# Kernel optimization log

Measured on AMD Instinct MI355X. Metric: run time of the kernel, lower is better.

## Reference

```python
import jax, jax.numpy as jnp
import numpy as np

B, C_IN, H, W = 4, 512, 188, 188
SHARED_CH = 64
NUM_CLASS = 3
M = 200
NUM_MAX = 500
STRIDE = 8
PCR = (-75.2, -75.2, -2.0, 75.2, 75.2, 4.0)
VOX = (0.1, 0.1, 0.15)
OUT_CH = (2, 1, 3, 2, 1, 3)  # center, center_z, dim, rot, iou, hm
MIN_RADIUS = 2.0
OVERLAP = 0.1
INIT_BIAS = -2.19


def conv3x3(x, w):
    return jax.lax.conv_general_dilated(x, w, (1, 1), 'SAME',
                                        dimension_numbers=('NCHW', 'OIHW', 'NCHW'))


def bn_relu(x, p):
    # p: [4, C] = gamma, beta, running_mean, running_var (inference-mode BN)
    g, b, m, v = p[0], p[1], p[2], p[3]
    scale = (g * jax.lax.rsqrt(v + 1e-5))[None, :, None, None]
    y = (x - m[None, :, None, None]) * scale + b[None, :, None, None]
    return jax.nn.relu(y)


def gaussian_radius(height, width, min_overlap):
    # Faithful to OpenPCDet centernet_utils.gaussian_radius
    b1 = height + width
    c1 = width * height * (1 - min_overlap) / (1 + min_overlap)
    sq1 = jnp.sqrt(jnp.maximum(b1 * b1 - 4.0 * c1, 0.0))
    r1 = (b1 + sq1) / 2.0
    b2 = 2.0 * (height + width)
    c2 = (1 - min_overlap) * width * height
    sq2 = jnp.sqrt(jnp.maximum(b2 * b2 - 16.0 * c2, 0.0))
    r2 = (b2 + sq2) / 2.0
    a3 = 4.0 * min_overlap
    b3 = -2.0 * min_overlap * (height + width)
    c3 = (min_overlap - 1.0) * width * height
    sq3 = jnp.sqrt(jnp.maximum(b3 * b3 - 4.0 * a3 * c3, 0.0))
    r3 = (b3 + sq3) / 2.0
    return jnp.minimum(jnp.minimum(r1, r2), r3)


def assign_targets(gt_boxes):
    # gt_boxes: [B, M, 8] = x, y, z, dx, dy, dz, heading, class(1..NUM_CLASS)
    x, y, z = gt_boxes[..., 0], gt_boxes[..., 1], gt_boxes[..., 2]
    dx, dy, dz = gt_boxes[..., 3], gt_boxes[..., 4], gt_boxes[..., 5]
    heading = gt_boxes[..., 6]
    cls = jax.lax.stop_gradient(gt_boxes[..., 7]).astype(jnp.int32)

    cx = jnp.clip((x - PCR[0]) / VOX[0] / STRIDE, 0.0, W - 0.5)  # [B,M]
    cy = jnp.clip((y - PCR[1]) / VOX[1] / STRIDE, 0.0, H - 0.5)
    cxi = jax.lax.stop_gradient(jnp.floor(cx)).astype(jnp.int32)  # .int() trunc == floor (>=0)
    cyi = jax.lax.stop_gradient(jnp.floor(cy)).astype(jnp.int32)

    dxp = dx / VOX[0] / STRIDE
    dyp = dy / VOX[1] / STRIDE
    r = gaussian_radius(dxp, dyp, OVERLAP)
    r = jnp.maximum(jnp.floor(jax.lax.stop_gradient(r)), MIN_RADIUS)  # clamp_min(r.int(), 2)
    sigma = (2.0 * r + 1.0) / 6.0
    valid = (dx > 0) & (dy > 0)  # [B,M]

    ox = jnp.arange(W, dtype=jnp.int32)[None, None, :] - cxi[..., None]  # [B,M,W]
    oy = jnp.arange(H, dtype=jnp.int32)[None, None, :] - cyi[..., None]  # [B,M,H]
    d2 = (oy.astype(jnp.float32) ** 2)[:, :, :, None] + (ox.astype(jnp.float32) ** 2)[:, :, None, :]
    g = jnp.exp(-d2 / (2.0 * sigma * sigma)[:, :, None, None])  # [B,M,H,W]
    win = (jnp.abs(oy)[:, :, :, None] <= r[:, :, None, None]) & \
          (jnp.abs(ox)[:, :, None, :] <= r[:, :, None, None])
    g = jnp.where(win & valid[:, :, None, None], g, 0.0)

    # per-class max-splat (draw_gaussian_to_heatmap uses torch.max overlap)
    heatmap = jnp.stack(
        [jnp.max(jnp.where((cls == c + 1)[:, :, None, None], g, 0.0), axis=1)
         for c in range(NUM_CLASS)], axis=1)  # [B,NUM_CLASS,H,W]

    vf = valid.astype(gt_boxes.dtype)
    vals = jnp.stack([cx - cxi.astype(cx.dtype), cy - cyi.astype(cy.dtype), z,
                      jnp.log(dx), jnp.log(dy), jnp.log(dz),
                      jnp.cos(heading), jnp.sin(heading)], axis=-1) * vf[..., None]
    target_boxes = jnp.zeros((B, NUM_MAX, 8), gt_boxes.dtype).at[:, :M].set(vals)
    ind_vals = (cyi * W + cxi) * valid.astype(jnp.int32)
    inds = jnp.zeros((B, NUM_MAX), jnp.int32).at[:, :M].set(ind_vals)
    mask = jnp.zeros((B, NUM_MAX), jnp.int32).at[:, :M].set(valid.astype(jnp.int32))
    return heatmap, target_boxes, inds, mask


def setup_inputs() -> dict:
    key = jax.random.key(0)
    ks = jax.random.split(key, 16)
    spatial_features = jax.random.normal(ks[0], (B, C_IN, H, W), jnp.float32)
    x = jax.random.uniform(ks[1], (B, M), minval=-70.0, maxval=70.0)
    y = jax.random.uniform(ks[2], (B, M), minval=-70.0, maxval=70.0)
    z = jax.random.uniform(ks[3], (B, M), minval=-1.0, maxval=1.0)
    dx = jax.random.uniform(ks[4], (B, M), minval=1.5, maxval=5.0)
    dy = jax.random.uniform(ks[5], (B, M), minval=1.5, maxval=5.0)
    dz = jax.random.uniform(ks[6], (B, M), minval=1.0, maxval=3.0)
    hd = jax.random.uniform(ks[7], (B, M), minval=-np.pi, maxval=np.pi)
    cls = jax.random.randint(ks[8], (B, M), 1, NUM_CLASS + 1).astype(jnp.float32)
    gt_boxes = jnp.stack([x, y, z, dx, dy, dz, hd, cls], axis=-1)

    def mk_bn(k, lead):
        kk = jax.random.split(k, 4)
        g = 1.0 + 0.1 * jax.random.normal(kk[0], lead + (SHARED_CH,))
        b = 0.1 * jax.random.normal(kk[1], lead + (SHARED_CH,))
        m = 0.1 * jax.random.normal(kk[2], lead + (SHARED_CH,))
        v = jax.random.uniform(kk[3], lead + (SHARED_CH,), minval=0.5, maxval=1.5)
        return jnp.stack([g, b, m, v], axis=len(lead))

    w_shared = jax.random.normal(ks[9], (SHARED_CH, C_IN, 3, 3)) * (1.0 / np.sqrt(C_IN * 9))
    bn_shared = mk_bn(ks[10], ())
    w1_heads = jax.random.normal(ks[11], (6, SHARED_CH, SHARED_CH, 3, 3)) * (1.0 / np.sqrt(SHARED_CH * 9))
    bn_heads = mk_bn(ks[12], (6,))
    w2_heads = jax.random.normal(ks[13], (6, 3, SHARED_CH, 3, 3)) * (1.0 / np.sqrt(SHARED_CH * 9))
    b2_heads = jnp.zeros((6, 3), jnp.float32).at[5].set(INIT_BIAS)  # hm branch bias = -2.19
    return {'spatial_features': spatial_features, 'gt_boxes': gt_boxes,
            'w_shared': w_shared, 'bn_shared': bn_shared,
            'w1_heads': w1_heads, 'bn_heads': bn_heads,
            'w2_heads': w2_heads, 'b2_heads': b2_heads}


def reference(spatial_features, gt_boxes, w_shared, bn_shared,
              w1_heads, bn_heads, w2_heads, b2_heads):
    shared = bn_relu(conv3x3(spatial_features, w_shared), bn_shared)  # [B,64,H,W]

    def branch(w1, bnp, w2, b2):
        h = bn_relu(conv3x3(shared, w1), bnp)
        return conv3x3(h, w2) + b2[None, :, None, None]  # [B,3,H,W] (out padded to 3)

    outs = jax.vmap(branch)(w1_heads, bn_heads, w2_heads, b2_heads)  # [6,B,3,H,W]
    head_out = jnp.concatenate([outs[i, :, :OUT_CH[i]] for i in range(6)], axis=1)  # [B,12,H,W]

    heatmap, target_boxes, inds, mask = assign_targets(gt_boxes)
    return head_out, heatmap, target_boxes, inds, mask
```

## Files before the change

kernel.cpp:

```cpp
#include <hip/hip_runtime.h>
#include <hip/hip_bf16.h>

#define HWD 188
#define NPX (HWD*HWD)
#define NB 4
#define CIN 512
#define CH 64
#define MBOX 200
#define NMAX 500

#define HEAD_SZ (NB*12*NPX)
#define HM_OFF  HEAD_SZ
#define TB_OFF  (HM_OFF + NB*3*NPX)
#define IND_OFF (TB_OFF + NB*NMAX*8)
#define MSK_OFF (IND_OFF + NB*NMAX)

typedef short sh8 __attribute__((ext_vector_type(8)));
typedef float f4 __attribute__((ext_vector_type(4)));
typedef unsigned short us4 __attribute__((ext_vector_type(4)));

__device__ __constant__ int d_cum[6]  = {0, 2, 3, 6, 8, 9};
__device__ __constant__ int d_outc[6] = {2, 1, 3, 2, 1, 3};

__device__ __forceinline__ unsigned short bf16_bits(float v) {
  union { __hip_bfloat16 h; unsigned short u; } cv;
  cv.h = __float2bfloat16(v);
  return cv.u;
}

__device__ __forceinline__ int xcd_swz(int bid, int grid) {
  return (bid & 7) * (grid >> 3) + (bid >> 3);
}

__global__ __launch_bounds__(256) void wprep(
    const float* __restrict__ ws_, const float* __restrict__ w1_,
    const float* __restrict__ w2_, unsigned short* __restrict__ w1b,
    unsigned short* __restrict__ w2b, unsigned short* __restrict__ w3b) {
  int e = blockIdx.x * 256 + threadIdx.x;
  const int N1 = 9 * 16 * 64 * 32;
  const int N2 = 6 * 9 * 64 * 64;
  const int N3 = 6 * 9 * 16 * 64;
  if (e < N1) {
    int icr = e & 31; int r1 = e >> 5;
    int oc = r1 & 63; int r2 = r1 >> 6;
    int icq = r2 & 15; int tap = r2 >> 4;
    w1b[e] = bf16_bits(ws_[(oc * 512 + icq * 32 + icr) * 9 + tap]);
  } else if (e < N1 + N2) {
    int f = e - N1;
    int h = f / (9 * 64 * 64); int r = f % (9 * 64 * 64);
    int tap = r / (64 * 64); int r2 = r % (64 * 64);
    int oc = r2 / 64; int ic = r2 % 64;
    w2b[f] = bf16_bits(w1_[((h * 64 + oc) * 64 + ic) * 9 + tap]);
  } else if (e < N1 + N2 + N3) {
    int f = e - N1 - N2;
    int h = f / (9 * 16 * 64); int r = f % (9 * 16 * 64);
    int tap = r / (16 * 64); int r2 = r % (16 * 64);
    int oc = r2 / 64; int ic = r2 % 64;
    float v = (oc < 3) ? w2_[((h * 3 + oc) * 64 + ic) * 9 + tap] : 0.f;
    w3b[f] = bf16_bits(v);
  }
}

#define C1_LDS (10*18*32)
__global__ __launch_bounds__(256, 4) void conv1_mfma(
    const float* __restrict__ sf,
    const unsigned short* __restrict__ wb,
    const float* __restrict__ bnp,
    unsigned short* __restrict__ outp) {
  __shared__ __align__(16) short s_in[2][C1_LDS];
  const int t = threadIdx.x;
  const int swz = xcd_swz(blockIdx.x, 1152);
  const int b = swz / 288;
  const int tt = swz % 288;
  const int y0 = (tt / 12) * 8, x0 = (tt % 12) * 16;
  const int w = t >> 6, lane = t & 63, ln = lane & 15, kg = lane >> 4;
  const int rg = w & 1, og = w >> 1;

  const bool st_act = (t < 240);
  const int icg = t & 3, cg = (t >> 2) % 6, sr = (t >> 2) / 6;
  const int gy_s = y0 - 1 + sr;
  const int gx0_s = x0 - 4 + cg * 4;
  const bool row_ok = (gy_s >= 0 && gy_s < HWD);
  const bool vec_ok = (gx0_s >= 0 && gx0_s + 3 < HWD);
  const float* sbase = sf + (((long long)b * CIN + icg * 8) * HWD + gy_s) * HWD + gx0_s;

  f4 acc[2][4];
#pragma unroll
  for (int i = 0; i < 2; ++i)
#pragma unroll
    for (int j = 0; j < 4; ++j) acc[i][j] = (f4){0.f, 0.f, 0.f, 0.f};

  f4 st[8];
#pragma unroll
  for (int j = 0; j < 8; ++j) st[j] = (f4){0.f, 0.f, 0.f, 0.f};

#define C1_LOAD(IC0)                                                        \
  do {                                                                      \
    if (st_act && row_ok) {                                                 \
      const float* p = sbase + (long long)(IC0) * NPX;                      \
      if (vec_ok) {                                                         \
        _Pragma("unroll")                                                   \
        for (int j = 0; j < 8; ++j)                                         \
          st[j] = *reinterpret_cast<const f4*>(p + (long long)j * NPX);     \
      } else {                                                              \
        _Pragma("unroll")                                                   \
        for (int j = 0; j < 8; ++j) st[j] = (f4){0.f, 0.f, 0.f, 0.f};       \
        _Pragma("unroll")                                                   \
        for (int k = 0; k < 4; ++k) {                                       \
          int gx = gx0_s + k;                                               \
          if (gx >= 0 && gx < HWD) {                                        \
            _Pragma("unroll")                                               \
            for (int j = 0; j < 8; ++j) st[j][k] = p[(long long)j * NPX + k];\
          }                                                                 \
        }                                                                   \
      }                                                                     \
    } else {                                                                \
      _Pragma("unroll")                                                     \
      for (int j = 0; j < 8; ++j) st[j] = (f4){0.f, 0.f, 0.f, 0.f};         \
    }                                                                       \
  } while (0)

#define C1_WRITE(BUF)                                                       \
  do {                                                                      \
    if (st_act) {                                                           \
      _Pragma("unroll")                                                     \
      for (int k = 0; k < 4; ++k) {                                         \
        int col = cg * 4 + k - 3;                                           \
        if ((unsigned)col < 18u) {                                          \
          sh8 pk;                                                           \
          _Pragma("unroll")                                                 \
          for (int j = 0; j < 8; ++j) pk[j] = (short)bf16_bits(st[j][k]);   \
          *reinterpret_cast<sh8*>(&(BUF)[(sr * 18 + col) * 32 + icg * 8]) = pk; \
        }                                                                   \
      }                                                                     \
    }                                                                       \
  } while (0)

  C1_LOAD(0);
  C1_WRITE(s_in[0]);
  __syncthreads();

  for (int s = 0; s < 16; ++s) {
    const short* cur = s_in[s & 1];
    if (s < 15) C1_LOAD((s + 1) * 32);
#pragma unroll
    for (int tap = 0; tap < 9; ++tap) {
      const int ky = tap / 3, kx = tap % 3;
      sh8 af[2];
#pragma unroll
      for (int i = 0; i < 2; ++i)
        af[i] = *reinterpret_cast<const sh8*>(
            wb + (((tap * 16 + s) * 64) + (2 * og + i) * 16 + ln) * 32 + kg * 8);
#pragma unroll
      for (int nt = 0; nt < 4; ++nt) {
        const int rr = 4 * rg + nt + ky;
        const int cc = ln + kx;
        sh8 bf = *reinterpret_cast<const sh8*>(&cur[(rr * 18 + cc) * 32 + kg * 8]);
#pragma unroll
        for (int i = 0; i < 2; ++i)
          acc[i][nt] = __builtin_amdgcn_mfma_f32_16x16x32_bf16(
              af[i], bf, acc[i][nt], 0, 0, 0);
      }
    }
    if (s < 15) C1_WRITE(s_in[(s & 1) ^ 1]);
    __syncthreads();
  }

#pragma unroll
  for (int i = 0; i < 2; ++i) {
    const int ocb = (2 * og + i) * 16 + kg * 4;
    f4 g4 = *reinterpret_cast<const f4*>(bnp + ocb);
    f4 b4 = *reinterpret_cast<const f4*>(bnp + 64 + ocb);
    f4 m4 = *reinterpret_cast<const f4*>(bnp + 128 + ocb);
    f4 v4 = *reinterpret_cast<const f4*>(bnp + 192 + ocb);
    f4 sc, bi;
#pragma unroll
    for (int j = 0; j < 4; ++j) {
      sc[j] = g4[j] * rsqrtf(v4[j] + 1e-5f);
      bi[j] = b4[j] - m4[j] * sc[j];
    }
#pragma unroll
    for (int nt = 0; nt < 4; ++nt) {
      int y = y0 + 4 * rg + nt;
      int x = x0 + ln;
      if (y < HWD && x < HWD) {
        us4 pk;
#pragma unroll
        for (int j = 0; j < 4; ++j)
          pk[j] = bf16_bits(fmaxf(acc[i][nt][j] * sc[j] + bi[j], 0.f));
        *reinterpret_cast<us4*>(outp + (((long long)b * HWD + y) * HWD + x) * 64 + ocb) = pk;
      }
    }
  }
#undef C1_LOAD
#undef C1_WRITE
}

__global__ __launch_bounds__(256, 3) void conv23_fused(
    const unsigned short* __restrict__ inp,
    const unsigned short* __restrict__ w2b,
    const unsigned short* __restrict__ w3b,
    const float* __restrict__ bnH,
    const float* __restrict__ b2,
    float* __restrict__ hout) {
  __shared__ __align__(16) short s_in[240 * 72];
  __shared__ __align__(16) short s_buf[180 * 36];
  const int t = threadIdx.x;
  const int swz = xcd_swz(blockIdx.x, 6912);
  const int h = swz % 6;
  const int tile = swz / 6;
  const int b = tile / 288;
  const int tt = tile % 288;
  const int y0 = (tt / 12) * 8, x0 = (tt % 12) * 16;
  const int w = t >> 6, lane = t & 63, ln = lane & 15, kg = lane >> 4;

  for (int idx = t; idx < 1920; idx += 256) {
    int ch8 = idx & 7; int px = idx >> 3;
    int r = (px * 205) >> 12; int c = px - r * 20;
    int gy = y0 - 2 + r, gx = x0 - 2 + c;
    sh8 v = (sh8){0, 0, 0, 0, 0, 0, 0, 0};
    if (gy >= 0 && gy < HWD && gx >= 0 && gx < HWD)
      v = *reinterpret_cast<const sh8*>(
          &inp[(((long long)b * HWD + gy) * HWD + gx) * 64 + ch8 * 8]);
    *reinterpret_cast<sh8*>(&s_in[px * 72 + ch8 * 8]) = v;
  }

  int ibase[3];
  int qaddr[3];
  bool wr_ok[3];
  bool img_ok[3];
#pragma unroll
  for (int nt = 0; nt < 3; ++nt) {
    int q = (w * 3 + nt) * 16 + ln;
    wr_ok[nt] = (q < 180);
    if (q > 179) q = 179;
    int r2 = (q * 57) >> 10; int c2 = q - r2 * 18;
    ibase[nt] = (r2 * 20 + c2) * 72 + kg * 8;
    qaddr[nt] = q;
    int gy2 = y0 - 1 + r2, gx2 = x0 - 1 + c2;
    img_ok[nt] = (gy2 >= 0 && gy2 < HWD && gx2 >= 0 && gx2 < HWD);
  }
  int b3base[2], oy[2], ox[2];
#pragma unroll
  for (int nt = 0; nt < 2; ++nt) {
    int p = (w * 2 + nt) * 16 + ln;
    int r3 = p >> 4, c3 = p & 15;
    b3base[nt] = ((r3 + 1) * 18 + (c3 + 1)) * 36 + kg * 8;
    oy[nt] = y0 + r3; ox[nt] = x0 + c3;
  }

  const float* bnp = bnH + h * 256;
  f4 acc3[2];
#pragma unroll
  for (int j = 0; j < 2; ++j) acc3[j] = (f4){0.f, 0.f, 0.f, 0.f};

  __syncthreads();

  for (int O = 0; O < 2; ++O) {
    f4 acc2[2][3];
#pragma unroll
    for (int i = 0; i < 2; ++i)
#pragma unroll
      for (int j = 0; j < 3; ++j) acc2[i][j] = (f4){0.f, 0.f, 0.f, 0.f};
    for (int icq = 0; icq < 2; ++icq) {
#pragma unroll
      for (int tap = 0; tap < 9; ++tap) {
        const int ky = tap / 3, kx = tap % 3;
        const int toff = (ky * 20 + kx) * 72 + icq * 32;
        sh8 af[2];
#pragma unroll
        for (int mt = 0; mt < 2; ++mt)
          af[mt] = *reinterpret_cast<const sh8*>(
              w2b + (((h * 9 + tap) * 64) + O * 32 + mt * 16 + ln) * 64 + icq * 32 + kg * 8);
#pragma unroll
        for (int nt = 0; nt < 3; ++nt) {
          sh8 bf = *reinterpret_cast<const sh8*>(&s_in[ibase[nt] + toff]);
#pragma unroll
          for (int mt = 0; mt < 2; ++mt)
            acc2[mt][nt] = __builtin_amdgcn_mfma_f32_16x16x32_bf16(
                af[mt], bf, acc2[mt][nt], 0, 0, 0);
        }
      }
    }
#pragma unroll
    for (int mt = 0; mt < 2; ++mt) {
      const int ocb = O * 32 + mt * 16 + kg * 4;
      f4 g4 = *reinterpret_cast<const f4*>(bnp + ocb);
      f4 b4 = *reinterpret_cast<const f4*>(bnp + 64 + ocb);
      f4 m4 = *reinterpret_cast<const f4*>(bnp + 128 + ocb);
      f4 v4 = *reinterpret_cast<const f4*>(bnp + 192 + ocb);
      f4 sc, bi;
#pragma unroll
      for (int j = 0; j < 4; ++j) {
        sc[j] = g4[j] * rsqrtf(v4[j] + 1e-5f);
        bi[j] = b4[j] - m4[j] * sc[j];
      }
#pragma unroll
      for (int nt = 0; nt < 3; ++nt) {
        if (wr_ok[nt]) {
          us4 pk = {0, 0, 0, 0};
          if (img_ok[nt]) {
#pragma unroll
            for (int j = 0; j < 4; ++j)
              pk[j] = bf16_bits(fmaxf(acc2[mt][nt][j] * sc[j] + bi[j], 0.f));
          }
          *reinterpret_cast<us4*>(&s_buf[qaddr[nt] * 36 + mt * 16 + kg * 4]) = pk;
        }
      }
    }
    __syncthreads();
#pragma unroll
    for (int tap = 0; tap < 9; ++tap) {
      const int dy = tap / 3 - 1, dx = tap % 3 - 1;
      const int toff = (dy * 18 + dx) * 36;
      sh8 af3 = *reinterpret_cast<const sh8*>(
          w3b + (((h * 9 + tap) * 16) + ln) * 64 + O * 32 + kg * 8);
#pragma unroll
      for (int nt = 0; nt < 2; ++nt) {
        sh8 bf3 = *reinterpret_cast<const sh8*>(&s_buf[b3base[nt] + toff]);
        acc3[nt] = __builtin_amdgcn_mfma_f32_16x16x32_bf16(af3, bf3, acc3[nt], 0, 0, 0);
      }
    }
    __syncthreads();
  }

  const int c_off = d_cum[h], noc = d_outc[h];
#pragma unroll
  for (int nt = 0; nt < 2; ++nt) {
    if (oy[nt] < HWD && ox[nt] < HWD) {
#pragma unroll
      for (int j = 0; j < 4; ++j) {
        int oc = kg * 4 + j;
        if (oc < noc)
          hout[((long long)b * 12 + c_off + oc) * NPX + oy[nt] * HWD + ox[nt]] =
              acc3[nt][j] + b2[h * 3 + oc];
      }
    }
  }
}

__global__ __launch_bounds__(256) void targets_kernel(
    const float* __restrict__ gt, float* __restrict__ out, float* __restrict__ boxp) {
  int idx = blockIdx.x * 256 + threadIdx.x;
  if (idx >= NB * NMAX) return;
  int b = idx / NMAX, j = idx - b * NMAX;
  float vals[8] = {0, 0, 0, 0, 0, 0, 0, 0};
  float indf = 0.f, mkf = 0.f;
  if (j < MBOX) {
    const float* g = gt + (b * MBOX + j) * 8;
    float x = g[0], y = g[1], z = g[2], dx = g[3], dy = g[4], dz = g[5];
    float hd = g[6], cls = g[7];
    float cx = (x - (-75.2f)) / 0.1f / 8.0f;
    cx = fminf(fmaxf(cx, 0.0f), (float)HWD - 0.5f);
    float cy = (y - (-75.2f)) / 0.1f / 8.0f;
    cy = fminf(fmaxf(cy, 0.0f), (float)HWD - 0.5f);
    float cxf = floorf(cx), cyf = floorf(cy);
    int cxi = (int)cxf, cyi = (int)cyf;
    float hh = dx / 0.1f / 8.0f;
    float ww = dy / 0.1f / 8.0f;
    const float ov = 0.1f;
    float b1 = hh + ww;
    float c1 = ww * hh * (1.0f - ov) / (1.0f + ov);
    float sq1 = sqrtf(fmaxf(b1 * b1 - 4.0f * c1, 0.0f));
    float r1 = (b1 + sq1) / 2.0f;
    float b2_ = 2.0f * (hh + ww);
    float c2 = (1.0f - ov) * ww * hh;
    float sq2 = sqrtf(fmaxf(b2_ * b2_ - 16.0f * c2, 0.0f));
    float r2 = (b2_ + sq2) / 2.0f;
    float a3 = 4.0f * ov;
    float b3 = -2.0f * ov * (hh + ww);
    float c3 = (ov - 1.0f) * ww * hh;
    float sq3 = sqrtf(fmaxf(b3 * b3 - 4.0f * a3 * c3, 0.0f));
    float r3 = (b3 + sq3) / 2.0f;
    float r = fminf(fminf(r1, r2), r3);
    r = fmaxf(floorf(r), 2.0f);
    float sigma = (2.0f * r + 1.0f) / 6.0f;
    float inv2s2 = 1.0f / (2.0f * sigma * sigma);
    bool valid = (dx > 0.0f) && (dy > 0.0f);
    float vf = valid ? 1.0f : 0.0f;
    vals[0] = (cx - cxf) * vf;
    vals[1] = (cy - cyf) * vf;
    vals[2] = z * vf;
    vals[3] = logf(dx) * vf;
    vals[4] = logf(dy) * vf;
    vals[5] = logf(dz) * vf;
    vals[6] = cosf(hd) * vf;
    vals[7] = sinf(hd) * vf;
    indf = (float)((cyi * HWD + cxi) * (valid ? 1 : 0));
    mkf = vf;
    float* bp = boxp + (b * MBOX + j) * 8;
    bp[0] = cxf; bp[1] = cyf; bp[2] = r; bp[3] = inv2s2;
    bp[4] = valid ? cls : 0.0f; bp[5] = 0.f; bp[6] = 0.f; bp[7] = 0.f;
  }
  float* tb = out + TB_OFF + (b * NMAX + j) * 8;
#pragma unroll
  for (int k = 0; k < 8; ++k) tb[k] = vals[k];
  out[IND_OFF + b * NMAX + j] = indf;
  out[MSK_OFF + b * NMAX + j] = mkf;
}

__global__ __launch_bounds__(256) void heatmap_kernel(
    const float* __restrict__ boxp, float* __restrict__ out) {
  __shared__ float s_bp[MBOX][5];
  const int t = threadIdx.x, b = blockIdx.y;
  for (int e = t; e < MBOX * 5; e += 256) {
    int j = e / 5, k = e - j * 5;
    s_bp[j][k] = boxp[(b * MBOX + j) * 8 + k];
  }
  __syncthreads();
  int p = blockIdx.x * 256 + t;
  if (p >= NPX) return;
  int y = p / HWD, x = p - y * HWD;
  float a0 = 0.f, a1 = 0.f, a2 = 0.f;
  for (int j = 0; j < MBOX; ++j) {
    int c = (int)s_bp[j][4];
    if (c == 0) continue;
    float ox = (float)x - s_bp[j][0];
    float oy = (float)y - s_bp[j][1];
    float r = s_bp[j][2];
    if (fabsf(ox) <= r && fabsf(oy) <= r) {
      float gg = expf(-(ox * ox + oy * oy) * s_bp[j][3]);
      if (c == 1) a0 = fmaxf(a0, gg);
      else if (c == 2) a1 = fmaxf(a1, gg);
      else a2 = fmaxf(a2, gg);
    }
  }
  int base = HM_OFF + (b * 3 * HWD + y) * HWD + x;
  out[base] = a0;
  out[base + NPX] = a1;
  out[base + 2 * NPX] = a2;
}

extern "C" void kernel_launch(void* const* d_in, const int* in_sizes, int n_in,
                              void* d_out, int out_size, void* d_ws, size_t ws_size,
                              hipStream_t stream) {
  (void)in_sizes; (void)n_in; (void)out_size; (void)ws_size;
  const float* sf = (const float*)d_in[0];
  const float* gt = (const float*)d_in[1];
  const float* w_shared = (const float*)d_in[2];
  const float* bn_shared = (const float*)d_in[3];
  const float* w1 = (const float*)d_in[4];
  const float* bnH = (const float*)d_in[5];
  const float* w2 = (const float*)d_in[6];
  const float* b2 = (const float*)d_in[7];
  float* out = (float*)d_out;
  char* ws = (char*)d_ws;

  const size_t SH = (size_t)NB * NPX * 64 * 2;
  unsigned short* shared_t = (unsigned short*)ws;
  unsigned short* w1b = (unsigned short*)(ws + SH);
  unsigned short* w2b = (unsigned short*)(ws + SH + 589824);
  unsigned short* w3b = (unsigned short*)(ws + SH + 589824 + 442368);
  float* boxp = (float*)(ws + SH + 589824 + 442368 + 110592);

  wprep<<<2232, 256, 0, stream>>>(w_shared, w1, w2, w1b, w2b, w3b);

  conv1_mfma<<<1152, 256, 0, stream>>>(sf, w1b, bn_shared, shared_t);

  conv23_fused<<<6912, 256, 0, stream>>>(shared_t, w2b, w3b, bnH, b2, out);

  targets_kernel<<<(NB * NMAX + 255) / 256, 256, 0, stream>>>(gt, out, boxp);
  heatmap_kernel<<<dim3((NPX + 255) / 256, NB), 256, 0, stream>>>(boxp, out);
}
```

Baseline: 594.8 us.

## Pad LDS pixel stride, batch weight loads, add setprio, drop trailing barrier

Changes the per-pixel LDS stride in conv1 (32→40 shorts) and in the conv2/3 intermediate buffer (36→40) so that MFMA operand reads hit fewer bank conflicts. In conv23 the per-tap weight global loads are hoisted into register arrays loaded ahead of each MFMA loop, and the O/icq loops are fully unrolled. s_setprio brackets the MFMA sections so waves in the compute phase get issue priority, and the final redundant barrier after the last O iteration is removed. The hoisted weight arrays raise VGPR pressure and may hurt occupancy at the 3-waves launch bound, and the larger padded strides use more LDS.

Measured after the change: 596.8 us. Within noise of the previous version (+0.3%).

```diff
diff --git a/kernel.cpp b/kernel.cpp
--- a/kernel.cpp
+++ b/kernel.cpp
@@ -61,7 +61,8 @@
   }
 }
 
-#define C1_LDS (10*18*32)
+#define C1_PXS 40
+#define C1_LDS (10*18*C1_PXS)
 __global__ __launch_bounds__(256, 4) void conv1_mfma(
     const float* __restrict__ sf,
     const unsigned short* __restrict__ wb,
@@ -130,7 +131,7 @@
           sh8 pk;                                                           \
           _Pragma("unroll")                                                 \
           for (int j = 0; j < 8; ++j) pk[j] = (short)bf16_bits(st[j][k]);   \
-          *reinterpret_cast<sh8*>(&(BUF)[(sr * 18 + col) * 32 + icg * 8]) = pk; \
+          *reinterpret_cast<sh8*>(&(BUF)[(sr * 18 + col) * C1_PXS + icg * 8]) = pk; \
         }                                                                   \
       }                                                                     \
     }                                                                       \
@@ -143,6 +144,7 @@
   for (int s = 0; s < 16; ++s) {
     const short* cur = s_in[s & 1];
     if (s < 15) C1_LOAD((s + 1) * 32);
+    __builtin_amdgcn_s_setprio(1);
 #pragma unroll
     for (int tap = 0; tap < 9; ++tap) {
       const int ky = tap / 3, kx = tap % 3;
@@ -155,13 +157,14 @@
       for (int nt = 0; nt < 4; ++nt) {
         const int rr = 4 * rg + nt + ky;
         const int cc = ln + kx;
-        sh8 bf = *reinterpret_cast<const sh8*>(&cur[(rr * 18 + cc) * 32 + kg * 8]);
+        sh8 bf = *reinterpret_cast<const sh8*>(&cur[(rr * 18 + cc) * C1_PXS + kg * 8]);
 #pragma unroll
         for (int i = 0; i < 2; ++i)
           acc[i][nt] = __builtin_amdgcn_mfma_f32_16x16x32_bf16(
               af[i], bf, acc[i][nt], 0, 0, 0);
       }
     }
+    __builtin_amdgcn_s_setprio(0);
     if (s < 15) C1_WRITE(s_in[(s & 1) ^ 1]);
     __syncthreads();
   }
@@ -196,6 +199,7 @@
 #undef C1_WRITE
 }
 
+#define SB_PXS 40
 __global__ __launch_bounds__(256, 3) void conv23_fused(
     const unsigned short* __restrict__ inp,
     const unsigned short* __restrict__ w2b,
@@ -204,7 +208,7 @@
     const float* __restrict__ b2,
     float* __restrict__ hout) {
   __shared__ __align__(16) short s_in[240 * 72];
-  __shared__ __align__(16) short s_buf[180 * 36];
+  __shared__ __align__(16) short s_buf[180 * SB_PXS];
   const int t = threadIdx.x;
   const int swz = xcd_swz(blockIdx.x, 6912);
   const int h = swz % 6;
@@ -225,10 +229,8 @@
     *reinterpret_cast<sh8*>(&s_in[px * 72 + ch8 * 8]) = v;
   }
 
-  int ibase[3];
-  int qaddr[3];
-  bool wr_ok[3];
-  bool img_ok[3];
+  int ibase[3], qaddr[3];
+  bool wr_ok[3], img_ok[3];
 #pragma unroll
   for (int nt = 0; nt < 3; ++nt) {
     int q = (w * 3 + nt) * 16 + ln;
@@ -245,7 +247,7 @@
   for (int nt = 0; nt < 2; ++nt) {
     int p = (w * 2 + nt) * 16 + ln;
     int r3 = p >> 4, c3 = p & 15;
-    b3base[nt] = ((r3 + 1) * 18 + (c3 + 1)) * 36 + kg * 8;
+    b3base[nt] = ((r3 + 1) * 18 + (c3 + 1)) * SB_PXS + kg * 8;
     oy[nt] = y0 + r3; ox[nt] = x0 + c3;
   }
 
@@ -256,31 +258,37 @@
 
   __syncthreads();
 
+#pragma unroll
   for (int O = 0; O < 2; ++O) {
     f4 acc2[2][3];
 #pragma unroll
     for (int i = 0; i < 2; ++i)
 #pragma unroll
       for (int j = 0; j < 3; ++j) acc2[i][j] = (f4){0.f, 0.f, 0.f, 0.f};
+#pragma unroll
     for (int icq = 0; icq < 2; ++icq) {
+      sh8 af[2][9];
+#pragma unroll
+      for (int tap = 0; tap < 9; ++tap)
+#pragma unroll
+        for (int mt = 0; mt < 2; ++mt)
+          af[mt][tap] = *reinterpret_cast<const sh8*>(
+              w2b + (((h * 9 + tap) * 64) + O * 32 + mt * 16 + ln) * 64 + icq * 32 + kg * 8);
+      __builtin_amdgcn_s_setprio(1);
 #pragma unroll
       for (int tap = 0; tap < 9; ++tap) {
         const int ky = tap / 3, kx = tap % 3;
         const int toff = (ky * 20 + kx) * 72 + icq * 32;
-        sh8 af[2];
-#pragma unroll
-        for (int mt = 0; mt < 2; ++mt)
-          af[mt] = *reinterpret_cast<const sh8*>(
-              w2b + (((h * 9 + tap) * 64) + O * 32 + mt * 16 + ln) * 64 + icq * 32 + kg * 8);
 #pragma unroll
         for (int nt = 0; nt < 3; ++nt) {
           sh8 bf = *reinterpret_cast<const sh8*>(&s_in[ibase[nt] + toff]);
 #pragma unroll
           for (int mt = 0; mt < 2; ++mt)
             acc2[mt][nt] = __builtin_amdgcn_mfma_f32_16x16x32_bf16(
-                af[mt], bf, acc2[mt][nt], 0, 0, 0);
+                af[mt][tap], bf, acc2[mt][nt], 0, 0, 0);
         }
       }
+      __builtin_amdgcn_s_setprio(0);
     }
 #pragma unroll
     for (int mt = 0; mt < 2; ++mt) {
@@ -304,24 +312,29 @@
             for (int j = 0; j < 4; ++j)
               pk[j] = bf16_bits(fmaxf(acc2[mt][nt][j] * sc[j] + bi[j], 0.f));
           }
-          *reinterpret_cast<us4*>(&s_buf[qaddr[nt] * 36 + mt * 16 + kg * 4]) = pk;
+          *reinterpret_cast<us4*>(&s_buf[qaddr[nt] * SB_PXS + mt * 16 + kg * 4]) = pk;
         }
       }
     }
     __syncthreads();
+    sh8 af3[9];
+#pragma unroll
+    for (int tap = 0; tap < 9; ++tap)
+      af3[tap] = *reinterpret_cast<const sh8*>(
+          w3b + (((h * 9 + tap) * 16) + ln) * 64 + O * 32 + kg * 8);
+    __builtin_amdgcn_s_setprio(1);
 #pragma unroll
     for (int tap = 0; tap < 9; ++tap) {
       const int dy = tap / 3 - 1, dx = tap % 3 - 1;
-      const int toff = (dy * 18 + dx) * 36;
-      sh8 af3 = *reinterpret_cast<const sh8*>(
-          w3b + (((h * 9 + tap) * 16) + ln) * 64 + O * 32 + kg * 8);
+      const int toff = (dy * 18 + dx) * SB_PXS;
 #pragma unroll
       for (int nt = 0; nt < 2; ++nt) {
         sh8 bf3 = *reinterpret_cast<const sh8*>(&s_buf[b3base[nt] + toff]);
-        acc3[nt] = __builtin_amdgcn_mfma_f32_16x16x32_bf16(af3, bf3, acc3[nt], 0, 0, 0);
-      }
-    }
-    __syncthreads();
+        acc3[nt] = __builtin_amdgcn_mfma_f32_16x16x32_bf16(af3[tap], bf3, acc3[nt], 0, 0, 0);
+      }
+    }
+    __builtin_amdgcn_s_setprio(0);
+    if (O == 0) __syncthreads();
   }
 
   const int c_off = d_cum[h], noc = d_outc[h];
```
